# Optimization experiments

Hardware: AMD Instinct MI355X
Metric: run time of the kernel (lower is better)

Reference implementation:

```python
import jax, jax.numpy as jnp
import numpy as np

EPS = 1e-6
N_NODES = 50000
N_EDGES = 800000
IN_DIM = 128
OUT_DIM = 128
HEADS = 4
D_K = OUT_DIM // HEADS
ATT_DIM = 2 * D_K + 1  # use_edge_feat=True


def setup_inputs() -> dict:
    key = jax.random.key(0)
    ks = jax.random.split(key, 8)
    h = jax.random.normal(ks[0], (N_NODES, IN_DIM), dtype=jnp.float32)
    edge_index = jax.random.randint(ks[1], (2, N_EDGES), 0, N_NODES, dtype=jnp.int64)
    edge_feat = jax.random.normal(ks[2], (N_EDGES, 1), dtype=jnp.float32)
    # parameters
    W_w = jax.random.normal(ks[3], (OUT_DIM, IN_DIM), dtype=jnp.float32) / np.sqrt(IN_DIM)
    W_b = jnp.zeros((OUT_DIM,), dtype=jnp.float32)
    att = jax.random.normal(ks[4], (HEADS, ATT_DIM), dtype=jnp.float32)
    ln_g = jnp.ones((OUT_DIM,), dtype=jnp.float32)
    ln_b = jnp.zeros((OUT_DIM,), dtype=jnp.float32)
    return {"h": h, "edge_index": edge_index, "edge_feat": edge_feat,
            "W_w": W_w, "W_b": W_b, "att": att, "ln_g": ln_g, "ln_b": ln_b}


def _layer_norm(x, g, b):
    mu = jnp.mean(x, axis=-1, keepdims=True)
    var = jnp.mean(jnp.square(x - mu), axis=-1, keepdims=True)
    return (x - mu) * jax.lax.rsqrt(var + 1e-5) * g + b


def reference(h, edge_index, edge_feat, W_w, W_b, att, ln_g, ln_b):
    num_nodes = h.shape[0]
    z = h @ W_w.T + W_b                      # [N, out_dim]
    zr = z.reshape(num_nodes, HEADS, D_K)    # [N, H, d_k]
    src, dst = edge_index[0], edge_index[1]
    h_s = zr[src]                            # [E, H, d_k]
    h_d = zr[dst]                            # [E, H, d_k]
    f_e = jnp.broadcast_to(edge_feat[:, None, :], (edge_feat.shape[0], HEADS, 1))
    concat = jnp.concatenate([h_s, h_d, f_e], axis=-1)  # [E, H, att_dim]
    scores = jnp.sum(concat * att[None], axis=-1)        # [E, H]
    scores = jnp.where(scores >= 0, scores, 0.2 * scores)  # LeakyReLU(0.2)
    scores = jnp.clip(scores, -20.0, 20.0)
    alpha = jnp.exp(scores)                               # [E, H]
    denom = jax.ops.segment_sum(alpha, dst, num_segments=num_nodes)  # [N, H]
    norm_alpha = alpha / (denom[dst] + EPS)               # [E, H]
    weighted = h_s * norm_alpha[..., None]                # [E, H, d_k]
    out = jax.ops.segment_sum(weighted, dst, num_segments=num_nodes)  # [N, H, d_k]
    out = out.reshape(num_nodes, OUT_DIM) + z
    out = _layer_norm(out, ln_g, ln_b)
    return jax.nn.elu(out)
```

## Files before the change

kernel.cpp:

```cpp
#include <hip/hip_runtime.h>
#include <hip/hip_bf16.h>
#include <math.h>

typedef __attribute__((ext_vector_type(8))) short bf16x8;
typedef __attribute__((ext_vector_type(4))) float f32x4;

__device__ __forceinline__ unsigned short f2bf(float f) {
    unsigned u = __float_as_uint(f);
    unsigned r = ((u >> 16) & 1u) + 0x7fffu;
    return (unsigned short)((u + r) >> 16);
}
__device__ __forceinline__ float bfL(unsigned u) { return __uint_as_float(u << 16); }
__device__ __forceinline__ float bfH(unsigned u) { return __uint_as_float(u & 0xffff0000u); }

#define SCORE_NPB 32

__global__ __launch_bounds__(256) void k_prep(const float* __restrict__ W,
                                              const float* __restrict__ bias,
                                              const float* __restrict__ att,
                                              const float* __restrict__ h,
                                              unsigned short* __restrict__ Wb16,
                                              float* __restrict__ s_src,
                                              float* __restrict__ s_dst,
                                              int* __restrict__ head8,
                                              int N, int scoreBlocks) {
    const int t = threadIdx.x;
    const int bid = blockIdx.x;
    if (bid == 0) {
#pragma unroll
        for (int q = 0; q < 8; ++q) {
            int gi = q * 256 + t;
            int kg = gi >> 7, row = gi & 127;
            int kbase = (kg >> 2) * 32 + (kg & 3) * 4;
            unsigned pk[4];
#pragma unroll
            for (int p = 0; p < 4; ++p) {
                int e0 = 2 * p, e1 = 2 * p + 1;
                float v0 = W[(size_t)row * 128 + kbase + (e0 >> 2) * 16 + (e0 & 3)];
                float v1 = W[(size_t)row * 128 + kbase + (e1 >> 2) * 16 + (e1 & 3)];
                pk[p] = ((unsigned)f2bf(v1) << 16) | f2bf(v0);
            }
            *reinterpret_cast<uint4*>(&Wb16[(size_t)gi * 8]) =
                make_uint4(pk[0], pk[1], pk[2], pk[3]);
        }
    } else if (bid <= scoreBlocks) {
        __shared__ float wsdL[2][4][128];
        __shared__ float cs[8];
#pragma unroll
        for (int q = 0; q < 4; ++q) {
            int idx = q * 256 + t;
            int isD = idx >> 9, rem = idx & 511;
            int hd = rem >> 7, k = rem & 127;
            float w = 0.f;
            for (int j = 0; j < 32; ++j)
                w += W[(size_t)(hd * 32 + j) * 128 + k] * att[hd * 65 + isD * 32 + j];
            wsdL[isD][hd][k] = w;
        }
        if (t < 8) {
            int chd = t & 3, cIsD = t >> 2;
            float c = 0.f;
            for (int j = 0; j < 32; ++j)
                c += bias[chd * 32 + j] * att[chd * 65 + cIsD * 32 + j];
            cs[t] = c;
        }
        __syncthreads();
        int node = (bid - 1) * SCORE_NPB + (t >> 3);
        int p = t & 7;
        if (node < N) {
            const float* hp = h + (size_t)node * 128 + p * 16;
            float ss[4] = {0.f, 0.f, 0.f, 0.f}, sd[4] = {0.f, 0.f, 0.f, 0.f};
#pragma unroll
            for (int q = 0; q < 4; ++q) {
                float4 hv = *reinterpret_cast<const float4*>(hp + q * 4);
#pragma unroll
                for (int hd = 0; hd < 4; ++hd) {
                    const float* wa = &wsdL[0][hd][p * 16 + q * 4];
                    const float* wb = &wsdL[1][hd][p * 16 + q * 4];
                    ss[hd] += hv.x * wa[0] + hv.y * wa[1] + hv.z * wa[2] + hv.w * wa[3];
                    sd[hd] += hv.x * wb[0] + hv.y * wb[1] + hv.z * wb[2] + hv.w * wb[3];
                }
            }
#pragma unroll
            for (int off = 1; off < 8; off <<= 1)
#pragma unroll
                for (int hd = 0; hd < 4; ++hd) {
                    ss[hd] += __shfl_xor(ss[hd], off);
                    sd[hd] += __shfl_xor(sd[hd], off);
                }
            if (p == 0) {
                *reinterpret_cast<float4*>(&s_src[(size_t)node * 4]) =
                    make_float4(ss[0] + cs[0], ss[1] + cs[1], ss[2] + cs[2], ss[3] + cs[3]);
                *reinterpret_cast<float4*>(&s_dst[(size_t)node * 4]) =
                    make_float4(sd[0] + cs[4], sd[1] + cs[5], sd[2] + cs[6], sd[3] + cs[7]);
            }
        }
    } else {
        int i = ((bid - 1 - scoreBlocks) * 256 + t) * 4;
        if (i < N * 8)
            *reinterpret_cast<int4*>(&head8[i]) = make_int4(-1, -1, -1, -1);
    }
}

__global__ __launch_bounds__(256) void k_work(
        const float* __restrict__ h, const unsigned short* __restrict__ Wb16,
        const float* __restrict__ bias, unsigned short* __restrict__ zb16,
        const int* __restrict__ src, const int* __restrict__ dst,
        const float* __restrict__ ef, const float* __restrict__ att,
        const float* __restrict__ s_src, const float* __restrict__ s_dst,
        int* __restrict__ head8, int4* __restrict__ epkt,
        int N, int E, int gemmBlocks) {
    __shared__ short hS[16 * 64 * 8];
    const int t = threadIdx.x;
    const int bid = blockIdx.x;

    if (bid >= gemmBlocks) {
        int e = (bid - gemmBlocks) * 256 + t;
        if (e >= E) return;
        int s = src[e], d = dst[e];
        float fv = ef[e];
        float4 ss = *reinterpret_cast<const float4*>(&s_src[(size_t)s * 4]);
        float4 sd = *reinterpret_cast<const float4*>(&s_dst[(size_t)d * 4]);
        float aE0 = att[64], aE1 = att[129], aE2 = att[194], aE3 = att[259];
        float sc0 = ss.x + sd.x + fv * aE0;
        float sc1 = ss.y + sd.y + fv * aE1;
        float sc2 = ss.z + sd.z + fv * aE2;
        float sc3 = ss.w + sd.w + fv * aE3;
        sc0 = sc0 >= 0.f ? sc0 : 0.2f * sc0;  sc1 = sc1 >= 0.f ? sc1 : 0.2f * sc1;
        sc2 = sc2 >= 0.f ? sc2 : 0.2f * sc2;  sc3 = sc3 >= 0.f ? sc3 : 0.2f * sc3;
        float a0 = expf(fminf(fmaxf(sc0, -20.f), 20.f));
        float a1 = expf(fminf(fmaxf(sc1, -20.f), 20.f));
        float a2 = expf(fminf(fmaxf(sc2, -20.f), 20.f));
        float a3 = expf(fminf(fmaxf(sc3, -20.f), 20.f));
        int prev = atomicExch(&head8[(size_t)d * 8 + (e & 7)], e);
        epkt[e] = make_int4(s, prev,
            (int)(((unsigned)f2bf(a1) << 16) | f2bf(a0)),
            (int)(((unsigned)f2bf(a3) << 16) | f2bf(a2)));
        return;
    }

    const int by = bid & 1;
    const int n0 = (bid >> 1) * 64;
    const int obase = by * 64;
#pragma unroll
    for (int q = 0; q < 8; ++q) {
        int f = q * 256 + t;
        int nd = f >> 5;
        int k4 = (f & 31) * 4;
        int ks = k4 >> 5, rr = k4 & 31;
        int half = rr >> 4, g = (rr & 15) >> 2;
        int kg = ks * 4 + g;
        int slot = kg * 64 + (nd ^ (kg & 7));
        int hn = n0 + nd; if (hn > N - 1) hn = N - 1;
        float4 v = *reinterpret_cast<const float4*>(&h[(size_t)hn * 128 + k4]);
        uint2 pk = make_uint2(((unsigned)f2bf(v.y) << 16) | f2bf(v.x),
                              ((unsigned)f2bf(v.w) << 16) | f2bf(v.z));
        *reinterpret_cast<uint2*>(&hS[slot * 8 + half * 4]) = pk;
    }
    __syncthreads();

    const int wv = t >> 6, l = t & 63;
    const int la = l & 15, lb = l >> 4;
    const int nbase = wv * 16;
    const int node = n0 + nbase + la;

    bf16x8 hfr[4];
#pragma unroll
    for (int ks = 0; ks < 4; ++ks) {
        int kg = ks * 4 + lb;
        int slot = kg * 64 + ((nbase + la) ^ (kg & 7));
        hfr[ks] = *reinterpret_cast<const bf16x8*>(&hS[slot * 8]);
    }

#pragma unroll
    for (int ot = 0; ot < 4; ++ot) {
        f32x4 acc = {0.f, 0.f, 0.f, 0.f};
#pragma unroll
        for (int ks = 0; ks < 4; ++ks) {
            int kg = ks * 4 + lb;
            bf16x8 wfr = *reinterpret_cast<const bf16x8*>(
                &Wb16[((size_t)kg * 128 + obase + ot * 16 + la) * 8]);
            acc = __builtin_amdgcn_mfma_f32_16x16x32_bf16(wfr, hfr[ks], acc, 0, 0, 0);
        }
        int colb = obase + ot * 16 + lb * 4;
        float4 bq = *reinterpret_cast<const float4*>(&bias[colb]);
        if (node < N) {
            uint2 pk = make_uint2(
                ((unsigned)f2bf(acc[1] + bq.y) << 16) | f2bf(acc[0] + bq.x),
                ((unsigned)f2bf(acc[3] + bq.w) << 16) | f2bf(acc[2] + bq.z));
            *reinterpret_cast<uint2*>(&zb16[(size_t)node * 128 + colb]) = pk;
        }
    }
}

__global__ __launch_bounds__(256) void k_agg_final(const int* __restrict__ head8,
                                                   const int4* __restrict__ epkt,
                                                   const uint4* __restrict__ zb4,
                                                   const float* __restrict__ g,
                                                   const float* __restrict__ bparm,
                                                   float* __restrict__ out, int N) {
    int wave = threadIdx.x >> 6, lane = threadIdx.x & 63;
    int l16 = lane & 15;
    int n = blockIdx.x * 16 + wave * 4 + (lane >> 4);
    if (n >= N) return;
    const int hd = l16 >> 2;
    int4 eha = *reinterpret_cast<const int4*>(&head8[(size_t)n * 8]);
    int4 ehb = *reinterpret_cast<const int4*>(&head8[(size_t)n * 8 + 4]);
    int e0 = eha.x, e1 = eha.y, e2 = eha.z, e3 = eha.w;
    int e4 = ehb.x, e5 = ehb.y, e6 = ehb.z, e7 = ehb.w;
    float A0 = 0.f, A1 = 0.f, A2 = 0.f, A3 = 0.f;
    float A4 = 0.f, A5 = 0.f, A6 = 0.f, A7 = 0.f;
    float da = 0.f;
#define UNPK(P, AV) { unsigned u = (hd & 2) ? (unsigned)(P).w : (unsigned)(P).z; \
    AV = (hd & 1) ? bfH(u) : bfL(u); }
#define STEP(EV) if (EV != -1) { \
        int4 p = epkt[EV]; \
        uint4 q = zb4[(size_t)p.x * 16 + l16]; \
        float a; UNPK(p, a) \
        A0 += bfL(q.x) * a; A1 += bfH(q.x) * a; \
        A2 += bfL(q.y) * a; A3 += bfH(q.y) * a; \
        A4 += bfL(q.z) * a; A5 += bfH(q.z) * a; \
        A6 += bfL(q.w) * a; A7 += bfH(q.w) * a; \
        da += a; EV = p.y; }
    while ((((e0 & e1) & (e2 & e3)) & ((e4 & e5) & (e6 & e7))) != -1) {
        STEP(e0) STEP(e1) STEP(e2) STEP(e3)
        STEP(e4) STEP(e5) STEP(e6) STEP(e7)
    }
#undef STEP
#undef UNPK

    float inv = 1.f / (da + 1e-6f);
    uint4 qz = zb4[(size_t)n * 16 + l16];
    float x0 = A0 * inv + bfL(qz.x);
    float x1 = A1 * inv + bfH(qz.x);
    float x2 = A2 * inv + bfL(qz.y);
    float x3 = A3 * inv + bfH(qz.y);
    float x4 = A4 * inv + bfL(qz.z);
    float x5 = A5 * inv + bfH(qz.z);
    float x6 = A6 * inv + bfL(qz.w);
    float x7 = A7 * inv + bfH(qz.w);
    float s = ((x0 + x1) + (x2 + x3)) + ((x4 + x5) + (x6 + x7));
#pragma unroll
    for (int off = 1; off < 16; off <<= 1) s += __shfl_xor(s, off);
    float mu = s * (1.f / 128.f);
    float d0 = x0 - mu, d1 = x1 - mu, d2 = x2 - mu, d3 = x3 - mu;
    float d4 = x4 - mu, d5 = x5 - mu, d6 = x6 - mu, d7 = x7 - mu;
    float q = ((d0 * d0 + d1 * d1) + (d2 * d2 + d3 * d3))
            + ((d4 * d4 + d5 * d5) + (d6 * d6 + d7 * d7));
#pragma unroll
    for (int off = 1; off < 16; off <<= 1) q += __shfl_xor(q, off);
    float rstd = rsqrtf(q * (1.f / 128.f) + 1e-5f);
    const int c = l16 * 8;
    float4 g0 = *reinterpret_cast<const float4*>(&g[c]);
    float4 g1 = *reinterpret_cast<const float4*>(&g[c + 4]);
    float4 b0 = *reinterpret_cast<const float4*>(&bparm[c]);
    float4 b1 = *reinterpret_cast<const float4*>(&bparm[c + 4]);
    float y0 = d0 * rstd * g0.x + b0.x;
    float y1 = d1 * rstd * g0.y + b0.y;
    float y2 = d2 * rstd * g0.z + b0.z;
    float y3 = d3 * rstd * g0.w + b0.w;
    float y4 = d4 * rstd * g1.x + b1.x;
    float y5 = d5 * rstd * g1.y + b1.y;
    float y6 = d6 * rstd * g1.z + b1.z;
    float y7 = d7 * rstd * g1.w + b1.w;
    y0 = y0 > 0.f ? y0 : expf(y0) - 1.f;
    y1 = y1 > 0.f ? y1 : expf(y1) - 1.f;
    y2 = y2 > 0.f ? y2 : expf(y2) - 1.f;
    y3 = y3 > 0.f ? y3 : expf(y3) - 1.f;
    y4 = y4 > 0.f ? y4 : expf(y4) - 1.f;
    y5 = y5 > 0.f ? y5 : expf(y5) - 1.f;
    y6 = y6 > 0.f ? y6 : expf(y6) - 1.f;
    y7 = y7 > 0.f ? y7 : expf(y7) - 1.f;
    *reinterpret_cast<float4*>(&out[(size_t)n * 128 + c]) = make_float4(y0, y1, y2, y3);
    *reinterpret_cast<float4*>(&out[(size_t)n * 128 + c + 4]) = make_float4(y4, y5, y6, y7);
}

extern "C" void kernel_launch(void* const* d_in, const int* in_sizes, int n_in,
                              void* d_out, int out_size, void* d_ws, size_t ws_size,
                              hipStream_t stream) {
    const float* h   = (const float*)d_in[0];
    const int*   ei  = (const int*)d_in[1];
    const float* ef  = (const float*)d_in[2];
    const float* Ww  = (const float*)d_in[3];
    const float* Wb  = (const float*)d_in[4];
    const float* att = (const float*)d_in[5];
    const float* lng = (const float*)d_in[6];
    const float* lnb = (const float*)d_in[7];
    float* out = (float*)d_out;

    const int N = in_sizes[0] / 128;
    const int E = in_sizes[1] / 2;
    const int* src = ei;
    const int* dst = ei + E;

    char* ws = (char*)d_ws;
    unsigned short* zb16   = (unsigned short*)ws; ws += (size_t)N * 128 * 2;
    unsigned short* Wb16   = (unsigned short*)ws; ws += (size_t)128 * 128 * 2;
    float*          s_src  = (float*)ws;          ws += (size_t)N * 4 * 4;
    float*          s_dst  = (float*)ws;          ws += (size_t)N * 4 * 4;
    int*            head8  = (int*)ws;            ws += (size_t)N * 8 * 4;
    int4*           epkt   = (int4*)ws;           ws += (size_t)E * 16;

    const int scoreBlocks = (N + SCORE_NPB - 1) / SCORE_NPB;
    const int headBlocks  = (N * 8 / 4 + 255) / 256;
    k_prep<<<1 + scoreBlocks + headBlocks, 256, 0, stream>>>(
        Ww, Wb, att, h, Wb16, s_src, s_dst, head8, N, scoreBlocks);

    const int gemmBlocks = ((N + 63) / 64) * 2;
    const int edgeBlocks = (E + 255) / 256;
    k_work<<<gemmBlocks + edgeBlocks, 256, 0, stream>>>(
        h, Wb16, Wb, zb16, src, dst, ef, att, s_src, s_dst, head8, epkt,
        N, E, gemmBlocks);
    k_agg_final<<<(N + 15) / 16, 256, 0, stream>>>(head8, epkt,
                                                   (const uint4*)zb16, lng, lnb, out, N);
}
```

Measured before the change: 125.5 us.

## Use four linked-list chains per node and eight lanes per node in aggregation

Each destination node now keeps four edge-list heads instead of eight, and the aggregation kernel gives each node 8 lanes that each handle 16 features instead of 16 lanes handling 8. Each block covers 32 nodes, so there are half as many lanes per node. Every lane issues two 16-byte loads per edge, and there are fewer redundant packet reads and shuffle-reduction steps. In exchange each chain is about twice as long, so more of the pointer chase runs serially, and each lane holds more accumulator registers.

```diff
diff --git a/kernel.cpp b/kernel.cpp
--- a/kernel.cpp
+++ b/kernel.cpp
@@ -22,7 +22,7 @@
                                               unsigned short* __restrict__ Wb16,
                                               float* __restrict__ s_src,
                                               float* __restrict__ s_dst,
-                                              int* __restrict__ head8,
+                                              int* __restrict__ head4,
                                               int N, int scoreBlocks) {
     const int t = threadIdx.x;
     const int bid = blockIdx.x;
@@ -96,8 +96,8 @@
         }
     } else {
         int i = ((bid - 1 - scoreBlocks) * 256 + t) * 4;
-        if (i < N * 8)
-            *reinterpret_cast<int4*>(&head8[i]) = make_int4(-1, -1, -1, -1);
+        if (i < N * 4)
+            *reinterpret_cast<int4*>(&head4[i]) = make_int4(-1, -1, -1, -1);
     }
 }
 
@@ -107,7 +107,7 @@
         const int* __restrict__ src, const int* __restrict__ dst,
         const float* __restrict__ ef, const float* __restrict__ att,
         const float* __restrict__ s_src, const float* __restrict__ s_dst,
-        int* __restrict__ head8, int4* __restrict__ epkt,
+        int* __restrict__ head4, int4* __restrict__ epkt,
         int N, int E, int gemmBlocks) {
     __shared__ short hS[16 * 64 * 8];
     const int t = threadIdx.x;
@@ -131,7 +131,7 @@
         float a1 = expf(fminf(fmaxf(sc1, -20.f), 20.f));
         float a2 = expf(fminf(fmaxf(sc2, -20.f), 20.f));
         float a3 = expf(fminf(fmaxf(sc3, -20.f), 20.f));
-        int prev = atomicExch(&head8[(size_t)d * 8 + (e & 7)], e);
+        int prev = atomicExch(&head4[(size_t)d * 4 + (e & 3)], e);
         epkt[e] = make_int4(s, prev,
             (int)(((unsigned)f2bf(a1) << 16) | f2bf(a0)),
             (int)(((unsigned)f2bf(a3) << 16) | f2bf(a2)));
@@ -192,86 +192,90 @@
     }
 }
 
-__global__ __launch_bounds__(256) void k_agg_final(const int* __restrict__ head8,
+__global__ __launch_bounds__(256) void k_agg_final(const int* __restrict__ head4,
                                                    const int4* __restrict__ epkt,
                                                    const uint4* __restrict__ zb4,
                                                    const float* __restrict__ g,
                                                    const float* __restrict__ bparm,
                                                    float* __restrict__ out, int N) {
     int wave = threadIdx.x >> 6, lane = threadIdx.x & 63;
-    int l16 = lane & 15;
-    int n = blockIdx.x * 16 + wave * 4 + (lane >> 4);
+    int l8 = lane & 7;
+    int n = blockIdx.x * 32 + wave * 8 + (lane >> 3);
     if (n >= N) return;
-    const int hd = l16 >> 2;
-    int4 eha = *reinterpret_cast<const int4*>(&head8[(size_t)n * 8]);
-    int4 ehb = *reinterpret_cast<const int4*>(&head8[(size_t)n * 8 + 4]);
-    int e0 = eha.x, e1 = eha.y, e2 = eha.z, e3 = eha.w;
-    int e4 = ehb.x, e5 = ehb.y, e6 = ehb.z, e7 = ehb.w;
-    float A0 = 0.f, A1 = 0.f, A2 = 0.f, A3 = 0.f;
-    float A4 = 0.f, A5 = 0.f, A6 = 0.f, A7 = 0.f;
+    const int hd = l8 >> 1;
+    int4 eh = *reinterpret_cast<const int4*>(&head4[(size_t)n * 4]);
+    int e0 = eh.x, e1 = eh.y, e2 = eh.z, e3 = eh.w;
+    float X0 = 0.f, X1 = 0.f, X2 = 0.f, X3 = 0.f;
+    float X4 = 0.f, X5 = 0.f, X6 = 0.f, X7 = 0.f;
+    float X8 = 0.f, X9 = 0.f, Xa = 0.f, Xb = 0.f;
+    float Xc = 0.f, Xd = 0.f, Xe = 0.f, Xf = 0.f;
     float da = 0.f;
 #define UNPK(P, AV) { unsigned u = (hd & 2) ? (unsigned)(P).w : (unsigned)(P).z; \
     AV = (hd & 1) ? bfH(u) : bfL(u); }
 #define STEP(EV) if (EV != -1) { \
         int4 p = epkt[EV]; \
-        uint4 q = zb4[(size_t)p.x * 16 + l16]; \
+        uint4 q0 = zb4[(size_t)p.x * 16 + l8 * 2]; \
+        uint4 q1 = zb4[(size_t)p.x * 16 + l8 * 2 + 1]; \
         float a; UNPK(p, a) \
-        A0 += bfL(q.x) * a; A1 += bfH(q.x) * a; \
-        A2 += bfL(q.y) * a; A3 += bfH(q.y) * a; \
-        A4 += bfL(q.z) * a; A5 += bfH(q.z) * a; \
-        A6 += bfL(q.w) * a; A7 += bfH(q.w) * a; \
+        X0 += bfL(q0.x) * a; X1 += bfH(q0.x) * a; \
+        X2 += bfL(q0.y) * a; X3 += bfH(q0.y) * a; \
+        X4 += bfL(q0.z) * a; X5 += bfH(q0.z) * a; \
+        X6 += bfL(q0.w) * a; X7 += bfH(q0.w) * a; \
+        X8 += bfL(q1.x) * a; X9 += bfH(q1.x) * a; \
+        Xa += bfL(q1.y) * a; Xb += bfH(q1.y) * a; \
+        Xc += bfL(q1.z) * a; Xd += bfH(q1.z) * a; \
+        Xe += bfL(q1.w) * a; Xf += bfH(q1.w) * a; \
         da += a; EV = p.y; }
-    while ((((e0 & e1) & (e2 & e3)) & ((e4 & e5) & (e6 & e7))) != -1) {
+    while (((e0 & e1) & (e2 & e3)) != -1) {
         STEP(e0) STEP(e1) STEP(e2) STEP(e3)
-        STEP(e4) STEP(e5) STEP(e6) STEP(e7)
     }
 #undef STEP
 #undef UNPK
 
     float inv = 1.f / (da + 1e-6f);
-    uint4 qz = zb4[(size_t)n * 16 + l16];
-    float x0 = A0 * inv + bfL(qz.x);
-    float x1 = A1 * inv + bfH(qz.x);
-    float x2 = A2 * inv + bfL(qz.y);
-    float x3 = A3 * inv + bfH(qz.y);
-    float x4 = A4 * inv + bfL(qz.z);
-    float x5 = A5 * inv + bfH(qz.z);
-    float x6 = A6 * inv + bfL(qz.w);
-    float x7 = A7 * inv + bfH(qz.w);
-    float s = ((x0 + x1) + (x2 + x3)) + ((x4 + x5) + (x6 + x7));
-#pragma unroll
-    for (int off = 1; off < 16; off <<= 1) s += __shfl_xor(s, off);
+    uint4 qz0 = zb4[(size_t)n * 16 + l8 * 2];
+    uint4 qz1 = zb4[(size_t)n * 16 + l8 * 2 + 1];
+    float x0 = X0 * inv + bfL(qz0.x), x1 = X1 * inv + bfH(qz0.x);
+    float x2 = X2 * inv + bfL(qz0.y), x3 = X3 * inv + bfH(qz0.y);
+    float x4 = X4 * inv + bfL(qz0.z), x5 = X5 * inv + bfH(qz0.z);
+    float x6 = X6 * inv + bfL(qz0.w), x7 = X7 * inv + bfH(qz0.w);
+    float x8 = X8 * inv + bfL(qz1.x), x9 = X9 * inv + bfH(qz1.x);
+    float xa = Xa * inv + bfL(qz1.y), xb = Xb * inv + bfH(qz1.y);
+    float xc = Xc * inv + bfL(qz1.z), xd = Xd * inv + bfH(qz1.z);
+    float xe = Xe * inv + bfL(qz1.w), xf = Xf * inv + bfH(qz1.w);
+    float s = (((x0 + x1) + (x2 + x3)) + ((x4 + x5) + (x6 + x7)))
+            + (((x8 + x9) + (xa + xb)) + ((xc + xd) + (xe + xf)));
+#pragma unroll
+    for (int off = 1; off < 8; off <<= 1) s += __shfl_xor(s, off);
     float mu = s * (1.f / 128.f);
     float d0 = x0 - mu, d1 = x1 - mu, d2 = x2 - mu, d3 = x3 - mu;
     float d4 = x4 - mu, d5 = x5 - mu, d6 = x6 - mu, d7 = x7 - mu;
-    float q = ((d0 * d0 + d1 * d1) + (d2 * d2 + d3 * d3))
-            + ((d4 * d4 + d5 * d5) + (d6 * d6 + d7 * d7));
-#pragma unroll
-    for (int off = 1; off < 16; off <<= 1) q += __shfl_xor(q, off);
+    float d8 = x8 - mu, d9 = x9 - mu, dA = xa - mu, dB = xb - mu;
+    float dC = xc - mu, dD = xd - mu, dE = xe - mu, dF = xf - mu;
+    float q = (((d0 * d0 + d1 * d1) + (d2 * d2 + d3 * d3))
+             + ((d4 * d4 + d5 * d5) + (d6 * d6 + d7 * d7)))
+            + (((d8 * d8 + d9 * d9) + (dA * dA + dB * dB))
+             + ((dC * dC + dD * dD) + (dE * dE + dF * dF)));
+#pragma unroll
+    for (int off = 1; off < 8; off <<= 1) q += __shfl_xor(q, off);
     float rstd = rsqrtf(q * (1.f / 128.f) + 1e-5f);
-    const int c = l16 * 8;
-    float4 g0 = *reinterpret_cast<const float4*>(&g[c]);
-    float4 g1 = *reinterpret_cast<const float4*>(&g[c + 4]);
-    float4 b0 = *reinterpret_cast<const float4*>(&bparm[c]);
-    float4 b1 = *reinterpret_cast<const float4*>(&bparm[c + 4]);
-    float y0 = d0 * rstd * g0.x + b0.x;
-    float y1 = d1 * rstd * g0.y + b0.y;
-    float y2 = d2 * rstd * g0.z + b0.z;
-    float y3 = d3 * rstd * g0.w + b0.w;
-    float y4 = d4 * rstd * g1.x + b1.x;
-    float y5 = d5 * rstd * g1.y + b1.y;
-    float y6 = d6 * rstd * g1.z + b1.z;
-    float y7 = d7 * rstd * g1.w + b1.w;
-    y0 = y0 > 0.f ? y0 : expf(y0) - 1.f;
-    y1 = y1 > 0.f ? y1 : expf(y1) - 1.f;
-    y2 = y2 > 0.f ? y2 : expf(y2) - 1.f;
-    y3 = y3 > 0.f ? y3 : expf(y3) - 1.f;
-    y4 = y4 > 0.f ? y4 : expf(y4) - 1.f;
-    y5 = y5 > 0.f ? y5 : expf(y5) - 1.f;
-    y6 = y6 > 0.f ? y6 : expf(y6) - 1.f;
-    y7 = y7 > 0.f ? y7 : expf(y7) - 1.f;
-    *reinterpret_cast<float4*>(&out[(size_t)n * 128 + c]) = make_float4(y0, y1, y2, y3);
-    *reinterpret_cast<float4*>(&out[(size_t)n * 128 + c + 4]) = make_float4(y4, y5, y6, y7);
+    const int c = l8 * 16;
+    float dv[16] = {d0, d1, d2, d3, d4, d5, d6, d7, d8, d9, dA, dB, dC, dD, dE, dF};
+#pragma unroll
+    for (int qb = 0; qb < 4; ++qb) {
+        float4 gg = *reinterpret_cast<const float4*>(&g[c + qb * 4]);
+        float4 bb = *reinterpret_cast<const float4*>(&bparm[c + qb * 4]);
+        float y0 = dv[qb * 4 + 0] * rstd * gg.x + bb.x;
+        float y1 = dv[qb * 4 + 1] * rstd * gg.y + bb.y;
+        float y2 = dv[qb * 4 + 2] * rstd * gg.z + bb.z;
+        float y3 = dv[qb * 4 + 3] * rstd * gg.w + bb.w;
+        y0 = y0 > 0.f ? y0 : expf(y0) - 1.f;
+        y1 = y1 > 0.f ? y1 : expf(y1) - 1.f;
+        y2 = y2 > 0.f ? y2 : expf(y2) - 1.f;
+        y3 = y3 > 0.f ? y3 : expf(y3) - 1.f;
+        *reinterpret_cast<float4*>(&out[(size_t)n * 128 + c + qb * 4]) =
+            make_float4(y0, y1, y2, y3);
+    }
 }
 
 extern "C" void kernel_launch(void* const* d_in, const int* in_sizes, int n_in,
@@ -297,19 +301,19 @@
     unsigned short* Wb16   = (unsigned short*)ws; ws += (size_t)128 * 128 * 2;
     float*          s_src  = (float*)ws;          ws += (size_t)N * 4 * 4;
     float*          s_dst  = (float*)ws;          ws += (size_t)N * 4 * 4;
-    int*            head8  = (int*)ws;            ws += (size_t)N * 8 * 4;
+    int*            head4  = (int*)ws;            ws += (size_t)N * 4 * 4;
     int4*           epkt   = (int4*)ws;           ws += (size_t)E * 16;
 
     const int scoreBlocks = (N + SCORE_NPB - 1) / SCORE_NPB;
-    const int headBlocks  = (N * 8 / 4 + 255) / 256;
+    const int headBlocks  = (N + 255) / 256;
     k_prep<<<1 + scoreBlocks + headBlocks, 256, 0, stream>>>(
-        Ww, Wb, att, h, Wb16, s_src, s_dst, head8, N, scoreBlocks);
+        Ww, Wb, att, h, Wb16, s_src, s_dst, head4, N, scoreBlocks);
 
     const int gemmBlocks = ((N + 63) / 64) * 2;
     const int edgeBlocks = (E + 255) / 256;
     k_work<<<gemmBlocks + edgeBlocks, 256, 0, stream>>>(
-        h, Wb16, Wb, zb16, src, dst, ef, att, s_src, s_dst, head8, epkt,
+        h, Wb16, Wb, zb16, src, dst, ef, att, s_src, s_dst, head4, epkt,
         N, E, gemmBlocks);
-    k_agg_final<<<(N + 15) / 16, 256, 0, stream>>>(head8, epkt,
+    k_agg_final<<<(N + 31) / 32, 256, 0, stream>>>(head4, epkt,
                                                    (const uint4*)zb16, lng, lnb, out, N);
 }
```

Result: faster. 116.7 us (-7.0%).
